# Kernel optimization log

Measured on AMD Instinct MI355X. Metric: run time of the kernel, lower is better.

Reference implementation:

```python
import jax, jax.numpy as jnp
import numpy as np
import math

GENE_E = 32
SUB_E = 768
HEAD_D = GENE_E // 2  # 16
DEPTH = 0
LAMBDA_INIT = 0.8 - 0.6 * math.exp(-0.3 * DEPTH)  # 0.2
EPS_SM = 1e-8
EPS_LN = 1e-5


def setup_inputs() -> dict:
    key = jax.random.key(0)
    ks = jax.random.split(key, 10)
    B, P, G, S = 8, 64, 128, 256
    return {
        "query": jax.random.normal(ks[0], (B, P, G, GENE_E), dtype=jnp.float32),
        "key": jax.random.normal(ks[1], (B, S, SUB_E), dtype=jnp.float32),
        "query_mask": jnp.ones((B, P, G), dtype=bool),
        "key_mask": jnp.ones((B, S), dtype=bool),
        "Wq": jax.random.normal(ks[2], (GENE_E, GENE_E), dtype=jnp.float32) * 0.05,
        "Wkv": jax.random.normal(ks[3], (2 * GENE_E, SUB_E), dtype=jnp.float32) * 0.02,
        "Wout": jax.random.normal(ks[4], (GENE_E, GENE_E), dtype=jnp.float32) * 0.05,
        "lambda_q1": jax.random.normal(ks[5], (HEAD_D,), dtype=jnp.float32) * 0.1,
        "lambda_k1": jax.random.normal(ks[6], (HEAD_D,), dtype=jnp.float32) * 0.1,
        "lambda_q2": jax.random.normal(ks[7], (HEAD_D,), dtype=jnp.float32) * 0.1,
        "lambda_k2": jax.random.normal(ks[8], (HEAD_D,), dtype=jnp.float32) * 0.1,
        "ln_weight": jnp.ones((GENE_E,), dtype=jnp.float32),
    }


def _stable_softmax(x, axis):
    x = x - jnp.max(x, axis=axis, keepdims=True)
    e = jnp.exp(x)
    return e / (jnp.sum(e, axis=axis, keepdims=True) + EPS_SM)


def _rmsnorm(x, w):
    var = jnp.mean(x * x, axis=-1, keepdims=True)
    return x * jax.lax.rsqrt(var + EPS_LN) * w


def reference(query, key, query_mask, key_mask, Wq, Wkv, Wout,
              lambda_q1, lambda_k1, lambda_q2, lambda_k2, ln_weight):
    B, P, G, E = query.shape
    S = key.shape[1]
    L = P * G
    scaling = HEAD_D ** -0.5

    gene_flat = query.reshape(B, L, E)
    Q = gene_flat @ Wq.T                      # [B, L, E]
    KV = key @ Wkv.T                          # [B, S, 2E]
    K, V = KV[..., :E], KV[..., E:]           # [B,S,E], [B,S,2h]==[B,S,E]

    Qh = Q.reshape(B, L, 2, HEAD_D).transpose(0, 2, 1, 3) * scaling  # [B,2,L,h]
    Kh = K.reshape(B, S, 2, HEAD_D).transpose(0, 2, 1, 3)            # [B,2,S,h]

    combined_mask = query_mask.reshape(B, L)[:, :, None] & key_mask[:, None, :]  # [B,L,S]

    scores = jnp.einsum('bnlh,bnsh->bnls', Qh, Kh)  # [B,2,L,S]
    scores = jnp.where(combined_mask[:, None], scores, -1e20)
    attn = _stable_softmax(scores, axis=-1)

    lam = (jnp.exp(jnp.sum(lambda_q1 * lambda_k1)) -
           jnp.exp(jnp.sum(lambda_q2 * lambda_k2)) + LAMBDA_INIT)

    diff = attn[:, 0] - lam * attn[:, 1]                 # [B,L,S]
    diff = diff - jnp.min(diff, axis=-1, keepdims=True) + 1e-20
    diff = jnp.where(combined_mask, diff, 0.0)

    attn_out = jnp.einsum('bls,bse->ble', diff, V)       # [B,L,2h]
    attn_out = _rmsnorm(attn_out, ln_weight) * (1.0 - LAMBDA_INIT)
    out = (attn_out @ Wout.T).reshape(B, P, G, E)
    return out, diff.reshape(B, P, G, S)
```

## Files before the change

### kernel.cpp

```cpp
#include <hip/hip_runtime.h>
#include <stdint.h>

typedef unsigned short u16;
typedef unsigned int u32;
typedef float f32x4 __attribute__((ext_vector_type(4)));
typedef short bf16x8 __attribute__((ext_vector_type(8)));

#define LL 8192
#define SS 256

__device__ __forceinline__ u32 pack_bf16(float lo, float hi) {
  return __builtin_amdgcn_perm(__float_as_uint(hi), __float_as_uint(lo), 0x07060302u);
}
__device__ __forceinline__ float rmax16(float v) {
  v = fmaxf(v, __shfl_xor(v, 1)); v = fmaxf(v, __shfl_xor(v, 2));
  v = fmaxf(v, __shfl_xor(v, 4)); v = fmaxf(v, __shfl_xor(v, 8)); return v;
}
__device__ __forceinline__ float rsum16(float v) {
  v += __shfl_xor(v, 1); v += __shfl_xor(v, 2);
  v += __shfl_xor(v, 4); v += __shfl_xor(v, 8); return v;
}
__device__ __forceinline__ float rmin16(float v) {
  v = fminf(v, __shfl_xor(v, 1)); v = fminf(v, __shfl_xor(v, 2));
  v = fminf(v, __shfl_xor(v, 4)); v = fminf(v, __shfl_xor(v, 8)); return v;
}

#define KV_LDS (24576 + 8192 + 2048)

__global__ __launch_bounds__(256, 2) void kv_kernel(
    const float* __restrict__ key, const float* __restrict__ Wkv,
    u16* __restrict__ K_bf, u16* __restrict__ Vt_bf) {
  extern __shared__ char smem[];
  float* keyS  = (float*)smem;
  float* parts = (float*)(smem + 24576);
  float* kvo   = (float*)(smem + 24576 + 8192);
  const int tid = threadIdx.x;
  const int w = tid >> 6, lane = tid & 63;
  const int b = blockIdx.x >> 5;
  const int s0 = (blockIdx.x & 31) * 8;

  u32 wr[24][4];
#pragma unroll
  for (int m = 0; m < 24; ++m) {
    const int ch = w * 24 + m;
    const float* src = Wkv + lane * 768 + ch * 8;
    float4 a = *(const float4*)src;
    float4 c = *(const float4*)(src + 4);
    wr[m][0] = pack_bf16(a.x, a.y); wr[m][1] = pack_bf16(a.z, a.w);
    wr[m][2] = pack_bf16(c.x, c.y); wr[m][3] = pack_bf16(c.z, c.w);
  }
  for (int i = 0; i < 6; ++i) {
    int idx = i * 256 + tid;
    int r = idx / 192;
    int off = idx - r * 192;
    float4 v = *(const float4*)(key + (size_t)(b * SS + s0 + r) * 768 + off * 4);
    *(float4*)(smem + idx * 16) = v;
  }
  __syncthreads();

  float acc[8] = {0.f, 0.f, 0.f, 0.f, 0.f, 0.f, 0.f, 0.f};
#pragma unroll
  for (int m = 0; m < 24; ++m) {
    const int ch = w * 24 + m;
    float wv[8];
#pragma unroll
    for (int p = 0; p < 4; ++p) {
      wv[2 * p]     = __uint_as_float(wr[m][p] << 16);
      wv[2 * p + 1] = __uint_as_float(wr[m][p] & 0xffff0000u);
    }
#pragma unroll
    for (int r = 0; r < 8; ++r) {
      const float* kp = keyS + r * 768 + ch * 8;
      float4 k0 = *(const float4*)kp;
      float4 k1 = *(const float4*)(kp + 4);
      acc[r] += wv[0] * k0.x + wv[1] * k0.y + wv[2] * k0.z + wv[3] * k0.w +
                wv[4] * k1.x + wv[5] * k1.y + wv[6] * k1.z + wv[7] * k1.w;
    }
  }
#pragma unroll
  for (int r = 0; r < 8; ++r) parts[(w * 8 + r) * 64 + lane] = acc[r];
  __syncthreads();
  for (int ii = 0; ii < 2; ++ii) {
    int o = tid + ii * 256;
    int r = o >> 6, eo = o & 63;
    kvo[r * 64 + eo] = parts[r * 64 + eo] + parts[512 + r * 64 + eo] +
                       parts[1024 + r * 64 + eo] + parts[1536 + r * 64 + eo];
  }
  __syncthreads();
  if (tid < 128) {
    int r = tid >> 4, i2 = tid & 15;
    const float* ko = kvo + r * 64 + 2 * i2;
    *(u32*)(K_bf + (size_t)(b * SS + s0 + r) * 32 + 2 * i2) = pack_bf16(ko[0], ko[1]);
  }
  {
    int e = tid >> 3, r = tid & 7;
    float v = kvo[r * 64 + 32 + e];
    Vt_bf[(size_t)(b * 32 + e) * SS + s0 + r] = (u16)(__float_as_uint(v) >> 16);
  }
}

#define MAIN_LDS 81920
#define OWQ   0
#define OWOUT 2048
#define OK    4096
#define OVT   24576
#define OWV   40960

__global__ __launch_bounds__(256, 2) void attn_kernel(
    const float* __restrict__ query,
    const u16* __restrict__ K_bf, const u16* __restrict__ Vt_bf,
    const float* __restrict__ Wq, const float* __restrict__ Wout,
    const float* __restrict__ lq1, const float* __restrict__ lk1,
    const float* __restrict__ lq2, const float* __restrict__ lk2,
    const float* __restrict__ lnw,
    float* __restrict__ out, float* __restrict__ diff) {
  extern __shared__ char smem[];
  const int tid = threadIdx.x;
  const int w = tid >> 6;
  const int gl = (tid >> 4) & 3;
  const int c = tid & 15;
  const int b = blockIdx.x >> 7;
  const int l0 = (blockIdx.x & 127) * 64;

#pragma unroll
  for (int i = 0; i < 4; ++i) {
    int o = i * 256 + tid;
    uint4 v = *(const uint4*)(K_bf + (size_t)b * 8192 + o * 8);
    *(uint4*)(smem + OK + (o >> 2) * 80 + (o & 3) * 16) = v;
  }
#pragma unroll
  for (int i = 0; i < 4; ++i) {
    int o = i * 256 + tid;
    uint4 v = *(const uint4*)(Vt_bf + (size_t)b * 8192 + o * 8);
    *(uint4*)(smem + OVT + ((o * 16) ^ (((o >> 5) & 31) << 4))) = v;
  }
  {
    const float SC = 0.36067376022224085f;
    float4 v = *(const float4*)(Wq + tid * 4);
    uint2 p; p.x = pack_bf16(v.x * SC, v.y * SC); p.y = pack_bf16(v.z * SC, v.w * SC);
    *(uint2*)(smem + OWQ + tid * 8) = p;
    float4 u = *(const float4*)(Wout + tid * 4);
    uint2 q; q.x = pack_bf16(u.x, u.y); q.y = pack_bf16(u.z, u.w);
    *(uint2*)(smem + OWOUT + tid * 8) = q;
  }
  float la1 = 0.f, la2 = 0.f;
#pragma unroll
  for (int i = 0; i < 16; ++i) { la1 += lq1[i] * lk1[i]; la2 += lq2[i] * lk2[i]; }
  const float lam = __expf(la1) - __expf(la2) + 0.2f;
  __syncthreads();

  char* wbase = smem + OWV + w * 10240;
  float* Qf = (float*)wbase;
  char* D2 = wbase + 2048;
  const int rowbase = b * LL + l0 + w * 16;

  bf16x8 ag;
  {
    const float* gp = query + (size_t)(rowbase + c) * 32 + gl * 8;
    float4 v0 = *(const float4*)gp;
    float4 v1 = *(const float4*)(gp + 4);
    union { u32 u[4]; bf16x8 v; } U;
    U.u[0] = pack_bf16(v0.x, v0.y); U.u[1] = pack_bf16(v0.z, v0.w);
    U.u[2] = pack_bf16(v1.x, v1.y); U.u[3] = pack_bf16(v1.z, v1.w);
    ag = U.v;
  }
#pragma unroll
  for (int t2 = 0; t2 < 2; ++t2) {
    bf16x8 bw = *(const bf16x8*)(smem + OWQ + (t2 * 16 + c) * 64 + gl * 16);
    f32x4 z = {0.f, 0.f, 0.f, 0.f};
    f32x4 q = __builtin_amdgcn_mfma_f32_16x16x32_bf16(ag, bw, z, 0, 0, 0);
#pragma unroll
    for (int j = 0; j < 4; ++j) Qf[(4 * gl + j) * 32 + t2 * 16 + c] = q[j];
  }

  bf16x8 aq[2];
#pragma unroll
  for (int h = 0; h < 2; ++h) {
    union { u32 u[4]; bf16x8 v; } U;
    if (gl < 2) {
      const float* qp = Qf + c * 32 + h * 16 + gl * 8;
      float4 v0 = *(const float4*)qp;
      float4 v1 = *(const float4*)(qp + 4);
      U.u[0] = pack_bf16(v0.x, v0.y); U.u[1] = pack_bf16(v0.z, v0.w);
      U.u[2] = pack_bf16(v1.x, v1.y); U.u[3] = pack_bf16(v1.z, v1.w);
    } else {
      U.u[0] = U.u[1] = U.u[2] = U.u[3] = 0u;
    }
    aq[h] = U.v;
  }
  f32x4 sc[2][16];
#pragma unroll
  for (int st = 0; st < 16; ++st) {
#pragma unroll
    for (int h = 0; h < 2; ++h) {
      bf16x8 bk = *(const bf16x8*)(smem + OK + (st * 16 + c) * 80 + h * 32 + (gl & 1) * 16);
      f32x4 z = {0.f, 0.f, 0.f, 0.f};
      sc[h][st] = __builtin_amdgcn_mfma_f32_16x16x32_bf16(aq[h], bk, z, 0, 0, 0);
    }
  }

#pragma unroll
  for (int j = 0; j < 4; ++j) {
    float m0 = sc[0][0][j], m1 = sc[1][0][j];
#pragma unroll
    for (int st = 1; st < 16; ++st) {
      m0 = fmaxf(m0, sc[0][st][j]); m1 = fmaxf(m1, sc[1][st][j]);
    }
    m0 = rmax16(m0); m1 = rmax16(m1);
    float s0 = 0.f, s1 = 0.f;
#pragma unroll
    for (int st = 0; st < 16; ++st) {
      float e0 = __builtin_amdgcn_exp2f(sc[0][st][j] - m0);
      float e1 = __builtin_amdgcn_exp2f(sc[1][st][j] - m1);
      sc[0][st][j] = e0; sc[1][st][j] = e1; s0 += e0; s1 += e1;
    }
    s0 = rsum16(s0); s1 = rsum16(s1);
    const float i0 = __builtin_amdgcn_rcpf(s0 + 1e-8f);
    const float i1 = __builtin_amdgcn_rcpf(s1 + 1e-8f) * lam;
    float mn = 0.f;
#pragma unroll
    for (int st = 0; st < 16; ++st) {
      float d = sc[0][st][j] * i0 - sc[1][st][j] * i1;
      sc[0][st][j] = d;
      mn = (st == 0) ? d : fminf(mn, d);
    }
    mn = rmin16(mn) - 1e-20f;
#pragma unroll
    for (int st = 0; st < 16; ++st) sc[0][st][j] -= mn;
  }

#pragma unroll
  for (int j = 0; j < 4; ++j) {
    const int r = 4 * gl + j;
    float* dp = diff + (size_t)(rowbase + r) * 256 + c;
    char* lp = D2 + r * 16 + (c & 7) * 2;
#pragma unroll
    for (int st = 0; st < 16; ++st) {
      float d = sc[0][st][j];
      dp[st * 16] = d;
      const int kc = st >> 1;
      const int g2 = ((st & 1) << 1) | (c >> 3);
      *(u16*)(lp + (kc * 4 + g2) * 256) = (u16)(__float_as_uint(d) >> 16);
    }
  }

  f32x4 ov0 = {0.f, 0.f, 0.f, 0.f}, ov1 = {0.f, 0.f, 0.f, 0.f};
#pragma unroll
  for (int kc = 0; kc < 8; ++kc) {
    bf16x8 ad = *(const bf16x8*)(D2 + (kc * 4 + gl) * 256 + c * 16);
    {
      const int e = c;
      bf16x8 bv = *(const bf16x8*)(smem + OVT + ((e * 512 + kc * 64 + gl * 16) ^ (e << 4)));
      ov0 = __builtin_amdgcn_mfma_f32_16x16x32_bf16(ad, bv, ov0, 0, 0, 0);
    }
    {
      const int e = 16 + c;
      bf16x8 bv = *(const bf16x8*)(smem + OVT + ((e * 512 + kc * 64 + gl * 16) ^ (e << 4)));
      ov1 = __builtin_amdgcn_mfma_f32_16x16x32_bf16(ad, bv, ov1, 0, 0, 0);
    }
  }

  const float ln0 = lnw[c], ln1 = lnw[16 + c];
#pragma unroll
  for (int j = 0; j < 4; ++j) {
    float ss = ov0[j] * ov0[j] + ov1[j] * ov1[j];
    ss = rsum16(ss);
    const float rs = __builtin_amdgcn_rsqf(ss * (1.0f / 32.0f) + 1e-5f) * 0.8f;
    Qf[(4 * gl + j) * 32 + c]      = ov0[j] * rs * ln0;
    Qf[(4 * gl + j) * 32 + 16 + c] = ov1[j] * rs * ln1;
  }

  bf16x8 ax;
  {
    const float* xp = Qf + c * 32 + gl * 8;
    float4 v0 = *(const float4*)xp;
    float4 v1 = *(const float4*)(xp + 4);
    union { u32 u[4]; bf16x8 v; } U;
    U.u[0] = pack_bf16(v0.x, v0.y); U.u[1] = pack_bf16(v0.z, v0.w);
    U.u[2] = pack_bf16(v1.x, v1.y); U.u[3] = pack_bf16(v1.z, v1.w);
    ax = U.v;
  }
#pragma unroll
  for (int t2 = 0; t2 < 2; ++t2) {
    bf16x8 bw = *(const bf16x8*)(smem + OWOUT + (t2 * 16 + c) * 64 + gl * 16);
    f32x4 z = {0.f, 0.f, 0.f, 0.f};
    f32x4 oc = __builtin_amdgcn_mfma_f32_16x16x32_bf16(ax, bw, z, 0, 0, 0);
#pragma unroll
    for (int j = 0; j < 4; ++j)
      out[(size_t)(rowbase + 4 * gl + j) * 32 + t2 * 16 + c] = oc[j];
  }
}

extern "C" void kernel_launch(void* const* d_in, const int* in_sizes, int n_in,
                              void* d_out, int out_size, void* d_ws, size_t ws_size,
                              hipStream_t stream) {
  const float* query = (const float*)d_in[0];
  const float* key   = (const float*)d_in[1];
  const float* Wq    = (const float*)d_in[4];
  const float* Wkv   = (const float*)d_in[5];
  const float* Wout  = (const float*)d_in[6];
  const float* lq1   = (const float*)d_in[7];
  const float* lk1   = (const float*)d_in[8];
  const float* lq2   = (const float*)d_in[9];
  const float* lk2   = (const float*)d_in[10];
  const float* lnw   = (const float*)d_in[11];
  float* out  = (float*)d_out;
  float* diff = out + (size_t)8 * 8192 * 32;
  u16* K_bf  = (u16*)d_ws;
  u16* Vt_bf = K_bf + 8 * 256 * 32;

  (void)hipFuncSetAttribute(reinterpret_cast<const void*>(kv_kernel),
                            hipFuncAttributeMaxDynamicSharedMemorySize, KV_LDS);
  (void)hipFuncSetAttribute(reinterpret_cast<const void*>(attn_kernel),
                            hipFuncAttributeMaxDynamicSharedMemorySize, MAIN_LDS);

  hipLaunchKernelGGL(kv_kernel, dim3(256), dim3(256), KV_LDS, stream,
                     key, Wkv, K_bf, Vt_bf);
  hipLaunchKernelGGL(attn_kernel, dim3(1024), dim3(256), MAIN_LDS, stream,
                     query, K_bf, Vt_bf, Wq, Wout, lq1, lk1, lq2, lk2, lnw, out, diff);
}
```

Baseline: 44.11 us.

## Restructure attention as single-wave blocks with transposed MFMA layout and direct K/V loads

Attention now runs as 4096 single-wavefront blocks that read K and V straight from global memory instead of staging whole tiles in LDS. The MFMA operands are swapped so scores come out transposed. This lets each lane write contiguous float4 rows of diff and out, and turns row reductions into two cross-lane shuffles. The two heads are computed one after the other, with the scaled head-1 probabilities kept packed as bf16 in registers to cut register pressure, at some loss of precision in the subtraction. The per-block setup cost and LDS footprint shrink, but every wave now does its own global reads of K, V, Wq and Wout and their bf16 conversion, relying on cache hits.

```diff
diff --git a/kernel.cpp b/kernel.cpp
--- a/kernel.cpp
+++ b/kernel.cpp
@@ -12,18 +12,14 @@
 __device__ __forceinline__ u32 pack_bf16(float lo, float hi) {
   return __builtin_amdgcn_perm(__float_as_uint(hi), __float_as_uint(lo), 0x07060302u);
 }
-__device__ __forceinline__ float rmax16(float v) {
-  v = fmaxf(v, __shfl_xor(v, 1)); v = fmaxf(v, __shfl_xor(v, 2));
-  v = fmaxf(v, __shfl_xor(v, 4)); v = fmaxf(v, __shfl_xor(v, 8)); return v;
-}
-__device__ __forceinline__ float rsum16(float v) {
-  v += __shfl_xor(v, 1); v += __shfl_xor(v, 2);
-  v += __shfl_xor(v, 4); v += __shfl_xor(v, 8); return v;
-}
-__device__ __forceinline__ float rmin16(float v) {
-  v = fminf(v, __shfl_xor(v, 1)); v = fminf(v, __shfl_xor(v, 2));
-  v = fminf(v, __shfl_xor(v, 4)); v = fminf(v, __shfl_xor(v, 8)); return v;
-}
+__device__ __forceinline__ bf16x8 pack8(float4 a, float4 b) {
+  union { u32 u[4]; bf16x8 v; } U;
+  U.u[0] = pack_bf16(a.x, a.y); U.u[1] = pack_bf16(a.z, a.w);
+  U.u[2] = pack_bf16(b.x, b.y); U.u[3] = pack_bf16(b.z, b.w);
+  return U.v;
+}
+__device__ __forceinline__ float bflo(u32 u) { return __uint_as_float(u << 16); }
+__device__ __forceinline__ float bfhi(u32 u) { return __uint_as_float(u & 0xffff0000u); }
 
 #define KV_LDS (24576 + 8192 + 2048)
 
@@ -99,14 +95,10 @@
   }
 }
 
-#define MAIN_LDS 81920
-#define OWQ   0
-#define OWOUT 2048
-#define OK    4096
-#define OVT   24576
-#define OWV   40960
-
-__global__ __launch_bounds__(256, 2) void attn_kernel(
+#define D2_STRIDE 528
+#define ATTN_LDS (16 * D2_STRIDE)
+
+__global__ __launch_bounds__(64, 3) void attn_kernel(
     const float* __restrict__ query,
     const u16* __restrict__ K_bf, const u16* __restrict__ Vt_bf,
     const float* __restrict__ Wq, const float* __restrict__ Wout,
@@ -115,179 +107,179 @@
     const float* __restrict__ lnw,
     float* __restrict__ out, float* __restrict__ diff) {
   extern __shared__ char smem[];
-  const int tid = threadIdx.x;
-  const int w = tid >> 6;
-  const int gl = (tid >> 4) & 3;
-  const int c = tid & 15;
-  const int b = blockIdx.x >> 7;
-  const int l0 = (blockIdx.x & 127) * 64;
-
-#pragma unroll
-  for (int i = 0; i < 4; ++i) {
-    int o = i * 256 + tid;
-    uint4 v = *(const uint4*)(K_bf + (size_t)b * 8192 + o * 8);
-    *(uint4*)(smem + OK + (o >> 2) * 80 + (o & 3) * 16) = v;
-  }
-#pragma unroll
-  for (int i = 0; i < 4; ++i) {
-    int o = i * 256 + tid;
-    uint4 v = *(const uint4*)(Vt_bf + (size_t)b * 8192 + o * 8);
-    *(uint4*)(smem + OVT + ((o * 16) ^ (((o >> 5) & 31) << 4))) = v;
-  }
-  {
-    const float SC = 0.36067376022224085f;
-    float4 v = *(const float4*)(Wq + tid * 4);
-    uint2 p; p.x = pack_bf16(v.x * SC, v.y * SC); p.y = pack_bf16(v.z * SC, v.w * SC);
-    *(uint2*)(smem + OWQ + tid * 8) = p;
-    float4 u = *(const float4*)(Wout + tid * 4);
-    uint2 q; q.x = pack_bf16(u.x, u.y); q.y = pack_bf16(u.z, u.w);
-    *(uint2*)(smem + OWOUT + tid * 8) = q;
-  }
+  const int lane = threadIdx.x;
+  const int gl = lane >> 4, c = lane & 15;
+  const int wid = blockIdx.x;
+  const int b = wid >> 9;
+  const int rowbase = b * LL + (wid & 511) * 16;
+  const u16* Kb = K_bf + (size_t)b * 8192;
+  const u16* Vb = Vt_bf + (size_t)b * 8192;
+
   float la1 = 0.f, la2 = 0.f;
 #pragma unroll
   for (int i = 0; i < 16; ++i) { la1 += lq1[i] * lk1[i]; la2 += lq2[i] * lk2[i]; }
   const float lam = __expf(la1) - __expf(la2) + 0.2f;
-  __syncthreads();
-
-  char* wbase = smem + OWV + w * 10240;
-  float* Qf = (float*)wbase;
-  char* D2 = wbase + 2048;
-  const int rowbase = b * LL + l0 + w * 16;
-
-  bf16x8 ag;
+
+  bf16x8 bgene;
   {
     const float* gp = query + (size_t)(rowbase + c) * 32 + gl * 8;
     float4 v0 = *(const float4*)gp;
     float4 v1 = *(const float4*)(gp + 4);
-    union { u32 u[4]; bf16x8 v; } U;
-    U.u[0] = pack_bf16(v0.x, v0.y); U.u[1] = pack_bf16(v0.z, v0.w);
-    U.u[2] = pack_bf16(v1.x, v1.y); U.u[3] = pack_bf16(v1.z, v1.w);
-    ag = U.v;
-  }
+    bgene = pack8(v0, v1);
+  }
+  u32 ph[2][2];
 #pragma unroll
   for (int t2 = 0; t2 < 2; ++t2) {
-    bf16x8 bw = *(const bf16x8*)(smem + OWQ + (t2 * 16 + c) * 64 + gl * 16);
+    const float SC = 0.36067376022224085f;
+    const float* wp = Wq + (size_t)(t2 * 16 + c) * 32 + gl * 8;
+    float4 a = *(const float4*)wp;
+    float4 d = *(const float4*)(wp + 4);
+    a.x *= SC; a.y *= SC; a.z *= SC; a.w *= SC;
+    d.x *= SC; d.y *= SC; d.z *= SC; d.w *= SC;
+    bf16x8 aw = pack8(a, d);
     f32x4 z = {0.f, 0.f, 0.f, 0.f};
-    f32x4 q = __builtin_amdgcn_mfma_f32_16x16x32_bf16(ag, bw, z, 0, 0, 0);
-#pragma unroll
-    for (int j = 0; j < 4; ++j) Qf[(4 * gl + j) * 32 + t2 * 16 + c] = q[j];
-  }
-
-  bf16x8 aq[2];
-#pragma unroll
-  for (int h = 0; h < 2; ++h) {
-    union { u32 u[4]; bf16x8 v; } U;
-    if (gl < 2) {
-      const float* qp = Qf + c * 32 + h * 16 + gl * 8;
-      float4 v0 = *(const float4*)qp;
-      float4 v1 = *(const float4*)(qp + 4);
-      U.u[0] = pack_bf16(v0.x, v0.y); U.u[1] = pack_bf16(v0.z, v0.w);
-      U.u[2] = pack_bf16(v1.x, v1.y); U.u[3] = pack_bf16(v1.z, v1.w);
-    } else {
-      U.u[0] = U.u[1] = U.u[2] = U.u[3] = 0u;
-    }
-    aq[h] = U.v;
-  }
-  f32x4 sc[2][16];
-#pragma unroll
-  for (int st = 0; st < 16; ++st) {
-#pragma unroll
-    for (int h = 0; h < 2; ++h) {
-      bf16x8 bk = *(const bf16x8*)(smem + OK + (st * 16 + c) * 80 + h * 32 + (gl & 1) * 16);
-      f32x4 z = {0.f, 0.f, 0.f, 0.f};
-      sc[h][st] = __builtin_amdgcn_mfma_f32_16x16x32_bf16(aq[h], bk, z, 0, 0, 0);
-    }
-  }
-
-#pragma unroll
-  for (int j = 0; j < 4; ++j) {
-    float m0 = sc[0][0][j], m1 = sc[1][0][j];
-#pragma unroll
-    for (int st = 1; st < 16; ++st) {
-      m0 = fmaxf(m0, sc[0][st][j]); m1 = fmaxf(m1, sc[1][st][j]);
-    }
-    m0 = rmax16(m0); m1 = rmax16(m1);
-    float s0 = 0.f, s1 = 0.f;
+    f32x4 qt = __builtin_amdgcn_mfma_f32_16x16x32_bf16(aw, bgene, z, 0, 0, 0);
+    ph[t2][0] = pack_bf16(qt[0], qt[1]);
+    ph[t2][1] = pack_bf16(qt[2], qt[3]);
+  }
+
+#define GATHER_QB(QB, H)                                                       \
+  {                                                                            \
+    int srcA = ((gl & 1) << 5) + c;                                            \
+    u32 w0 = (u32)__shfl((int)ph[H][0], srcA);                                 \
+    u32 w1 = (u32)__shfl((int)ph[H][1], srcA);                                 \
+    u32 w2 = (u32)__shfl((int)ph[H][0], srcA + 16);                            \
+    u32 w3 = (u32)__shfl((int)ph[H][1], srcA + 16);                            \
+    if (gl >= 2) { w0 = 0; w1 = 0; w2 = 0; w3 = 0; }                           \
+    union { u32 u[4]; bf16x8 v; } UU;                                          \
+    UU.u[0] = w0; UU.u[1] = w1; UU.u[2] = w2; UU.u[3] = w3;                    \
+    QB = UU.v;                                                                 \
+  }
+
+#define SCORE_HEAD(H, QB)                                                      \
+  {                                                                            \
+    _Pragma("unroll")                                                          \
+    for (int st = 0; st < 16; ++st) {                                          \
+      uint4 kf = {0u, 0u, 0u, 0u};                                             \
+      if (gl < 2)                                                              \
+        kf = *(const uint4*)(Kb + (size_t)(st * 16 + c) * 32 + (H) * 16 + gl * 8); \
+      union { uint4 u; bf16x8 v; } AA; AA.u = kf;                              \
+      f32x4 z = {0.f, 0.f, 0.f, 0.f};                                          \
+      sc[st] = __builtin_amdgcn_mfma_f32_16x16x32_bf16(AA.v, QB, z, 0, 0, 0);  \
+    }                                                                          \
+  }
+
+#define SOFTMAX(INV, EXTRA)                                                    \
+  {                                                                            \
+    f32x4 mq = sc[0];                                                          \
+    _Pragma("unroll")                                                          \
+    for (int st = 1; st < 16; ++st) {                                          \
+      mq[0] = fmaxf(mq[0], sc[st][0]); mq[1] = fmaxf(mq[1], sc[st][1]);        \
+      mq[2] = fmaxf(mq[2], sc[st][2]); mq[3] = fmaxf(mq[3], sc[st][3]);        \
+    }                                                                          \
+    float m = fmaxf(fmaxf(mq[0], mq[1]), fmaxf(mq[2], mq[3]));                 \
+    m = fmaxf(m, __shfl_xor(m, 16));                                           \
+    m = fmaxf(m, __shfl_xor(m, 32));                                           \
+    f32x4 sq = {0.f, 0.f, 0.f, 0.f};                                           \
+    _Pragma("unroll")                                                          \
+    for (int st = 0; st < 16; ++st) {                                          \
+      f32x4 e;                                                                 \
+      e[0] = __builtin_amdgcn_exp2f(sc[st][0] - m);                            \
+      e[1] = __builtin_amdgcn_exp2f(sc[st][1] - m);                            \
+      e[2] = __builtin_amdgcn_exp2f(sc[st][2] - m);                            \
+      e[3] = __builtin_amdgcn_exp2f(sc[st][3] - m);                            \
+      sc[st] = e;                                                              \
+      sq[0] += e[0]; sq[1] += e[1]; sq[2] += e[2]; sq[3] += e[3];              \
+    }                                                                          \
+    float s = (sq[0] + sq[1]) + (sq[2] + sq[3]);                               \
+    s += __shfl_xor(s, 16);                                                    \
+    s += __shfl_xor(s, 32);                                                    \
+    INV = __builtin_amdgcn_rcpf(s + 1e-8f) EXTRA;                              \
+  }
+
+  f32x4 sc[16];
+  u32 a1p[16][2];
+
+  {
+    bf16x8 qb1; GATHER_QB(qb1, 1);
+    SCORE_HEAD(1, qb1);
+    float i1;
+    SOFTMAX(i1, * lam);
 #pragma unroll
     for (int st = 0; st < 16; ++st) {
-      float e0 = __builtin_amdgcn_exp2f(sc[0][st][j] - m0);
-      float e1 = __builtin_amdgcn_exp2f(sc[1][st][j] - m1);
-      sc[0][st][j] = e0; sc[1][st][j] = e1; s0 += e0; s1 += e1;
-    }
-    s0 = rsum16(s0); s1 = rsum16(s1);
-    const float i0 = __builtin_amdgcn_rcpf(s0 + 1e-8f);
-    const float i1 = __builtin_amdgcn_rcpf(s1 + 1e-8f) * lam;
-    float mn = 0.f;
+      a1p[st][0] = pack_bf16(sc[st][0] * i1, sc[st][1] * i1);
+      a1p[st][1] = pack_bf16(sc[st][2] * i1, sc[st][3] * i1);
+    }
+  }
+
+  {
+    bf16x8 qb0; GATHER_QB(qb0, 0);
+    SCORE_HEAD(0, qb0);
+    float i0;
+    SOFTMAX(i0, );
+    f32x4 mn = {0.f, 0.f, 0.f, 0.f};
 #pragma unroll
     for (int st = 0; st < 16; ++st) {
-      float d = sc[0][st][j] * i0 - sc[1][st][j] * i1;
-      sc[0][st][j] = d;
-      mn = (st == 0) ? d : fminf(mn, d);
-    }
-    mn = rmin16(mn) - 1e-20f;
-#pragma unroll
-    for (int st = 0; st < 16; ++st) sc[0][st][j] -= mn;
-  }
-
-#pragma unroll
-  for (int j = 0; j < 4; ++j) {
-    const int r = 4 * gl + j;
-    float* dp = diff + (size_t)(rowbase + r) * 256 + c;
-    char* lp = D2 + r * 16 + (c & 7) * 2;
+      f32x4 d;
+      d[0] = sc[st][0] * i0 - bflo(a1p[st][0]);
+      d[1] = sc[st][1] * i0 - bfhi(a1p[st][0]);
+      d[2] = sc[st][2] * i0 - bflo(a1p[st][1]);
+      d[3] = sc[st][3] * i0 - bfhi(a1p[st][1]);
+      sc[st] = d;
+      if (st == 0) mn = d;
+      else {
+        mn[0] = fminf(mn[0], d[0]); mn[1] = fminf(mn[1], d[1]);
+        mn[2] = fminf(mn[2], d[2]); mn[3] = fminf(mn[3], d[3]);
+      }
+    }
+    float mns = fminf(fminf(mn[0], mn[1]), fminf(mn[2], mn[3]));
+    mns = fminf(mns, __shfl_xor(mns, 16));
+    mns = fminf(mns, __shfl_xor(mns, 32));
+    mns -= 1e-20f;
+    float* drow = diff + (size_t)(rowbase + c) * 256;
 #pragma unroll
     for (int st = 0; st < 16; ++st) {
-      float d = sc[0][st][j];
-      dp[st * 16] = d;
-      const int kc = st >> 1;
-      const int g2 = ((st & 1) << 1) | (c >> 3);
-      *(u16*)(lp + (kc * 4 + g2) * 256) = (u16)(__float_as_uint(d) >> 16);
+      f32x4 d;
+      d[0] = sc[st][0] - mns; d[1] = sc[st][1] - mns;
+      d[2] = sc[st][2] - mns; d[3] = sc[st][3] - mns;
+      *(f32x4*)(drow + st * 16 + 4 * gl) = d;
+      uint2 p; p.x = pack_bf16(d[0], d[1]); p.y = pack_bf16(d[2], d[3]);
+      *(uint2*)(smem + c * D2_STRIDE + st * 32 + gl * 8) = p;
     }
   }
 
   f32x4 ov0 = {0.f, 0.f, 0.f, 0.f}, ov1 = {0.f, 0.f, 0.f, 0.f};
 #pragma unroll
   for (int kc = 0; kc < 8; ++kc) {
-    bf16x8 ad = *(const bf16x8*)(D2 + (kc * 4 + gl) * 256 + c * 16);
-    {
-      const int e = c;
-      bf16x8 bv = *(const bf16x8*)(smem + OVT + ((e * 512 + kc * 64 + gl * 16) ^ (e << 4)));
-      ov0 = __builtin_amdgcn_mfma_f32_16x16x32_bf16(ad, bv, ov0, 0, 0, 0);
-    }
-    {
-      const int e = 16 + c;
-      bf16x8 bv = *(const bf16x8*)(smem + OVT + ((e * 512 + kc * 64 + gl * 16) ^ (e << 4)));
-      ov1 = __builtin_amdgcn_mfma_f32_16x16x32_bf16(ad, bv, ov1, 0, 0, 0);
-    }
+    bf16x8 ad = *(const bf16x8*)(smem + c * D2_STRIDE + kc * 64 + gl * 16);
+    bf16x8 bv0 = *(const bf16x8*)(Vb + (size_t)c * 256 + kc * 32 + gl * 8);
+    bf16x8 bv1 = *(const bf16x8*)(Vb + (size_t)(16 + c) * 256 + kc * 32 + gl * 8);
+    ov0 = __builtin_amdgcn_mfma_f32_16x16x32_bf16(ad, bv0, ov0, 0, 0, 0);
+    ov1 = __builtin_amdgcn_mfma_f32_16x16x32_bf16(ad, bv1, ov1, 0, 0, 0);
   }
 
   const float ln0 = lnw[c], ln1 = lnw[16 + c];
 #pragma unroll
   for (int j = 0; j < 4; ++j) {
     float ss = ov0[j] * ov0[j] + ov1[j] * ov1[j];
-    ss = rsum16(ss);
+    ss += __shfl_xor(ss, 1); ss += __shfl_xor(ss, 2);
+    ss += __shfl_xor(ss, 4); ss += __shfl_xor(ss, 8);
     const float rs = __builtin_amdgcn_rsqf(ss * (1.0f / 32.0f) + 1e-5f) * 0.8f;
-    Qf[(4 * gl + j) * 32 + c]      = ov0[j] * rs * ln0;
-    Qf[(4 * gl + j) * 32 + 16 + c] = ov1[j] * rs * ln1;
-  }
-
-  bf16x8 ax;
-  {
-    const float* xp = Qf + c * 32 + gl * 8;
-    float4 v0 = *(const float4*)xp;
-    float4 v1 = *(const float4*)(xp + 4);
-    union { u32 u[4]; bf16x8 v; } U;
-    U.u[0] = pack_bf16(v0.x, v0.y); U.u[1] = pack_bf16(v0.z, v0.w);
-    U.u[2] = pack_bf16(v1.x, v1.y); U.u[3] = pack_bf16(v1.z, v1.w);
-    ax = U.v;
-  }
+    u16* xrow = (u16*)(smem + (4 * gl + j) * 80);
+    xrow[c]      = (u16)(__float_as_uint(ov0[j] * rs * ln0) >> 16);
+    xrow[16 + c] = (u16)(__float_as_uint(ov1[j] * rs * ln1) >> 16);
+  }
+
+  bf16x8 xb = *(const bf16x8*)(smem + c * 80 + gl * 16);
 #pragma unroll
   for (int t2 = 0; t2 < 2; ++t2) {
-    bf16x8 bw = *(const bf16x8*)(smem + OWOUT + (t2 * 16 + c) * 64 + gl * 16);
+    const float* wp = Wout + (size_t)(t2 * 16 + c) * 32 + gl * 8;
+    float4 a = *(const float4*)wp;
+    float4 d2 = *(const float4*)(wp + 4);
+    bf16x8 aw = pack8(a, d2);
     f32x4 z = {0.f, 0.f, 0.f, 0.f};
-    f32x4 oc = __builtin_amdgcn_mfma_f32_16x16x32_bf16(ax, bw, z, 0, 0, 0);
-#pragma unroll
-    for (int j = 0; j < 4; ++j)
-      out[(size_t)(rowbase + 4 * gl + j) * 32 + t2 * 16 + c] = oc[j];
+    f32x4 oc = __builtin_amdgcn_mfma_f32_16x16x32_bf16(aw, xb, z, 0, 0, 0);
+    *(f32x4*)(out + (size_t)(rowbase + c) * 32 + t2 * 16 + 4 * gl) = oc;
   }
 }
 
@@ -309,13 +301,8 @@
   u16* K_bf  = (u16*)d_ws;
   u16* Vt_bf = K_bf + 8 * 256 * 32;
 
-  (void)hipFuncSetAttribute(reinterpret_cast<const void*>(kv_kernel),
-                            hipFuncAttributeMaxDynamicSharedMemorySize, KV_LDS);
-  (void)hipFuncSetAttribute(reinterpret_cast<const void*>(attn_kernel),
-                            hipFuncAttributeMaxDynamicSharedMemorySize, MAIN_LDS);
-
   hipLaunchKernelGGL(kv_kernel, dim3(256), dim3(256), KV_LDS, stream,
                      key, Wkv, K_bf, Vt_bf);
-  hipLaunchKernelGGL(attn_kernel, dim3(1024), dim3(256), MAIN_LDS, stream,
+  hipLaunchKernelGGL(attn_kernel, dim3(4096), dim3(64), ATTN_LDS, stream,
                      query, K_bf, Vt_bf, Wq, Wout, lq1, lk1, lq2, lk2, lnw, out, diff);
 }
```

Result: slower. 58.83 us (+33.4%).
